# Performance work log

Hardware: AMD Instinct MI355X
Metric: run time of the kernel (lower is better)

Reference implementation:

```python
import jax, jax.numpy as jnp
import numpy as np

N_POINTS = 32768
N_PRIMS = 2048
C_LIGHT = 299792458.0


def setup_inputs() -> dict:
    key = jax.random.key(0)
    k1, k2, k3, k4, k5 = jax.random.split(key, 5)
    # query points and primitive centers in a ~room-scale scene (metres)
    query_points = jax.random.normal(k1, (N_POINTS, 3), dtype=jnp.float32) * 2.0
    positions = jax.random.normal(k2, (N_PRIMS, 3), dtype=jnp.float32) * 2.0
    # diagonal anisotropic scales, kept away from zero for stability
    scales = jax.random.uniform(k3, (N_PRIMS, 3), dtype=jnp.float32, minval=0.1, maxval=1.0)
    amplitudes = jax.random.uniform(k4, (N_PRIMS,), dtype=jnp.float32, minval=0.0, maxval=1.0)
    phases = jax.random.uniform(k5, (N_PRIMS,), dtype=jnp.float32, minval=-np.pi, maxval=np.pi)
    return {
        "query_points": query_points,
        "positions": positions,
        "scales": scales,
        "amplitudes": amplitudes,
        "phases": phases,
        "frequency": 2400000000,  # 2.4 GHz
    }


def reference(query_points, positions, scales, amplitudes, phases, frequency):
    """Batched equivalent of: field = sum_p primitive_p.evaluate(query_points, frequency).

    Each complex Gaussian primitive contributes
        a_p * exp(-0.5 * (x-mu_p)^T diag(1/s_p^2) (x-mu_p)) * exp(i*(phi_p + k*|x-mu_p|))
    with wavenumber k = 2*pi*f/c. All pairwise terms are expressed as GEMMs.
    """
    f = jnp.float32(frequency)
    k_wave = jnp.float32(2.0 * np.pi) * f / jnp.float32(C_LIGHT)

    inv_var = 1.0 / (scales * scales)                      # [P,3]
    x2 = query_points * query_points                       # [N,3]
    mu2w = jnp.sum(positions * positions * inv_var, axis=1)  # [P]
    # Mahalanobis distance^2: sum_d (x_d-mu_d)^2 / s_d^2, expanded into GEMMs
    maha = (x2 @ inv_var.T
            - 2.0 * (query_points @ (positions * inv_var).T)
            + mu2w[None, :])                               # [N,P]
    maha = jnp.maximum(maha, 0.0)
    # Euclidean distance for the propagation phase
    d2 = (jnp.sum(x2, axis=1, keepdims=True)
          - 2.0 * (query_points @ positions.T)
          + jnp.sum(positions * positions, axis=1)[None, :])  # [N,P]
    r = jnp.sqrt(jnp.maximum(d2, 1e-12))

    w = amplitudes[None, :] * jnp.exp(-0.5 * maha)         # [N,P] real envelope
    ph = phases[None, :] + k_wave * r                      # [N,P] total phase
    field = jax.lax.complex(jnp.sum(w * jnp.cos(ph), axis=1),
                            jnp.sum(w * jnp.sin(ph), axis=1))  # [N] complex64
    return field
```

## Files before the change

kernel.cpp:

```cpp
#include <hip/hip_runtime.h>
#include <math.h>

#define NPOINTS 32768
#define NPRIMS  2048
#define BLK     256
#define PBLK    (NPOINTS / BLK)
#define NSPLIT  16

typedef float v2f __attribute__((ext_vector_type(2)));

struct PrimPair { float4 q0, q1, q2, q3; };

__device__ __forceinline__ float read_freq(const void* p) {
    const unsigned* w = (const unsigned*)p;
    unsigned lo = w[0];
    float ff = __uint_as_float(lo);
    if (ff >= 1.0e5f && ff <= 1.0e13f) return ff;
    if (lo != 0u) return (float)lo;
    double d = *(const double*)p;
    if (d >= 1.0e5 && d <= 1.0e13) return (float)d;
    unsigned long long v = ((unsigned long long)w[1] << 32) | lo;
    return (float)v;
}

__global__ __launch_bounds__(BLK) void prep_kernel(
        const float* __restrict__ pos,
        const float* __restrict__ scl,
        const float* __restrict__ amp,
        const float* __restrict__ ph,
        PrimPair* __restrict__ pp) {
    int j = blockIdx.x * blockDim.x + threadIdx.x;
    if (j >= NPRIMS / 2) return;
    const float KE     = -0.72134752044448169f;
    const float INV2PI =  0.15915494309189535f;
    int p0 = 2 * j, p1 = 2 * j + 1;
    float s0x = scl[3*p0+0], s0y = scl[3*p0+1], s0z = scl[3*p0+2];
    float s1x = scl[3*p1+0], s1y = scl[3*p1+1], s1z = scl[3*p1+2];
    PrimPair P;
    P.q0 = make_float4(pos[3*p0+0], pos[3*p1+0], pos[3*p0+1], pos[3*p1+1]);
    P.q1 = make_float4(pos[3*p0+2], pos[3*p1+2], amp[p0], amp[p1]);
    P.q2 = make_float4(KE / (s0x*s0x), KE / (s1x*s1x), KE / (s0y*s0y), KE / (s1y*s1y));
    P.q3 = make_float4(KE / (s0z*s0z), KE / (s1z*s1z), ph[p0] * INV2PI, ph[p1] * INV2PI);
    pp[j] = P;
}

__global__ __launch_bounds__(BLK) void field_kernel(
        const float* __restrict__ qp,
        const PrimPair* __restrict__ pp,
        const void* __restrict__ freq_p,
        float2* __restrict__ part) {
    const int n = blockIdx.x * BLK + threadIdx.x;
    const float x = qp[3*n+0], y = qp[3*n+1], z = qp[3*n+2];
    const float kr = read_freq(freq_p) / 299792458.0f;

    constexpr int PAIRS = (NPRIMS / NSPLIT) / 2;
    const int base = blockIdx.y * PAIRS;

    v2f re = {0.0f, 0.0f}, im = {0.0f, 0.0f};
    const v2f xx = {x, x}, yy = {y, y}, zz = {z, z};
    const v2f kr2 = {kr, kr};
    const v2f eps2 = {1e-12f, 1e-12f};

    #pragma unroll 4
    for (int j = 0; j < PAIRS; ++j) {
        PrimPair P = pp[base + j];
        v2f mux = {P.q0.x, P.q0.y}, muy = {P.q0.z, P.q0.w};
        v2f muz = {P.q1.x, P.q1.y}, am2 = {P.q1.z, P.q1.w};
        v2f gx  = {P.q2.x, P.q2.y}, gy  = {P.q2.z, P.q2.w};
        v2f gz  = {P.q3.x, P.q3.y}, ph2 = {P.q3.z, P.q3.w};

        v2f dx = xx - mux, dy = yy - muy, dz = zz - muz;
        v2f t0 = dx * dx, t1 = dy * dy, t2 = dz * dz;
        v2f e  = t0 * gx + t1 * gy + t2 * gz;
        v2f d2 = t0 + t1 + t2;
        d2 = __builtin_elementwise_max(d2, eps2);

        float r0 = __builtin_amdgcn_sqrtf(d2.x);
        float r1 = __builtin_amdgcn_sqrtf(d2.y);
        float e0 = __builtin_amdgcn_exp2f(e.x);
        float e1 = __builtin_amdgcn_exp2f(e.y);
        v2f r2 = {r0, r1};
        v2f ex = {e0, e1};
        v2f w2 = am2 * ex;
        v2f tp = kr2 * r2 + ph2;
        float f0 = __builtin_amdgcn_fractf(tp.x);
        float f1 = __builtin_amdgcn_fractf(tp.y);
        float s0 = __builtin_amdgcn_sinf(f0);
        float s1 = __builtin_amdgcn_sinf(f1);
        float c0 = __builtin_amdgcn_cosf(f0);
        float c1 = __builtin_amdgcn_cosf(f1);
        v2f s2 = {s0, s1}, c2 = {c0, c1};
        re += w2 * c2;
        im += w2 * s2;
    }

    part[(size_t)blockIdx.y * NPOINTS + n] = make_float2(re.x + re.y, im.x + im.y);
}

__global__ __launch_bounds__(BLK) void reduce_kernel(const float2* __restrict__ part,
                                                     float* __restrict__ out) {
    int n = blockIdx.x * blockDim.x + threadIdx.x;
    float re = 0.0f, im = 0.0f;
    #pragma unroll
    for (int s = 0; s < NSPLIT; ++s) {
        float2 v = part[(size_t)s * NPOINTS + n];
        re += v.x; im += v.y;
    }
    out[n]           = re;
    out[NPOINTS + n] = im;
}

__global__ __launch_bounds__(BLK) void field_fallback(
        const float* __restrict__ qp,
        const float* __restrict__ pos,
        const float* __restrict__ scl,
        const float* __restrict__ amp,
        const float* __restrict__ ph,
        const void*  __restrict__ freq_p,
        float*       __restrict__ out) {
    __shared__ float4 sA[128];
    __shared__ float4 sB[128];
    const int n = blockIdx.x * BLK + threadIdx.x;
    const float x = qp[3*n+0], y = qp[3*n+1], z = qp[3*n+2];
    const float kr = read_freq(freq_p) / 299792458.0f;
    const float KE = -0.72134752044448169f, INV2PI = 0.15915494309189535f;
    float re = 0.0f, im = 0.0f;
    for (int tile = 0; tile < NPRIMS / 128; ++tile) {
        __syncthreads();
        if (threadIdx.x < 128) {
            int p = tile * 128 + threadIdx.x;
            float sx = scl[3*p+0], sy = scl[3*p+1], sz = scl[3*p+2];
            sA[threadIdx.x] = make_float4(pos[3*p+0], pos[3*p+1], pos[3*p+2], amp[p]);
            sB[threadIdx.x] = make_float4(KE/(sx*sx), KE/(sy*sy), KE/(sz*sz), ph[p]*INV2PI);
        }
        __syncthreads();
        #pragma unroll 8
        for (int p = 0; p < 128; ++p) {
            float4 a = sA[p];
            float4 b = sB[p];
            float dx = x - a.x, dy = y - a.y, dz = z - a.z;
            float t0 = dx*dx, t1 = dy*dy, t2 = dz*dz;
            float e  = fmaf(t0, b.x, fmaf(t1, b.y, t2 * b.z));
            float d2 = t0 + t1 + t2;
            float r  = __builtin_amdgcn_sqrtf(fmaxf(d2, 1e-12f));
            float w  = a.w * __builtin_amdgcn_exp2f(e);
            float tp = __builtin_amdgcn_fractf(fmaf(kr, r, b.w));
            float s  = __builtin_amdgcn_sinf(tp);
            float c  = __builtin_amdgcn_cosf(tp);
            re = fmaf(w, c, re);
            im = fmaf(w, s, im);
        }
    }
    out[n]           = re;
    out[NPOINTS + n] = im;
}

extern "C" void kernel_launch(void* const* d_in, const int* in_sizes, int n_in,
                              void* d_out, int out_size, void* d_ws, size_t ws_size,
                              hipStream_t stream) {
    const float* qp  = (const float*)d_in[0];
    const float* pos = (const float*)d_in[1];
    const float* scl = (const float*)d_in[2];
    const float* amp = (const float*)d_in[3];
    const float* ph  = (const float*)d_in[4];
    const void*  fq  = d_in[5];
    float* out = (float*)d_out;

    const size_t packed_bytes = (size_t)(NPRIMS / 2) * sizeof(PrimPair);
    const size_t part_bytes   = (size_t)NSPLIT * NPOINTS * sizeof(float2);

    if (ws_size >= packed_bytes + part_bytes) {
        PrimPair* pp   = (PrimPair*)d_ws;
        float2*   part = (float2*)((char*)d_ws + packed_bytes);
        prep_kernel<<<dim3((NPRIMS/2 + BLK - 1) / BLK), dim3(BLK), 0, stream>>>(pos, scl, amp, ph, pp);
        field_kernel<<<dim3(PBLK, NSPLIT), dim3(BLK), 0, stream>>>(qp, pp, fq, part);
        reduce_kernel<<<dim3(NPOINTS / BLK), dim3(BLK), 0, stream>>>(part, out);
    } else {
        field_fallback<<<dim3(PBLK), dim3(BLK), 0, stream>>>(qp, pos, scl, amp, ph, fq, out);
    }
}
```

Before: 47.27 us.

## Process two points per thread and replace hardware sin/cos with packed polynomials

Each thread now evaluates two query points against each primitive pair, reusing every loaded PrimPair across both points and halving the grid. The hardware transcendental sin/cos (fract plus v_sin/v_cos on the quarter-rate unit) is replaced by packed minimax polynomials in revolutions, evaluated with packed FMA on full-rate ALUs. The next PrimPair is software-prefetched one iteration ahead. The trade-off is more registers, fewer waves in the grid, and more VALU instructions per term, with a possible small accuracy change from the polynomial.

```diff
diff --git a/kernel.cpp b/kernel.cpp
--- a/kernel.cpp
+++ b/kernel.cpp
@@ -4,7 +4,9 @@
 #define NPOINTS 32768
 #define NPRIMS  2048
 #define BLK     256
-#define PBLK    (NPOINTS / BLK)
+#define PPT     2
+#define PTS_BLK (BLK * PPT)
+#define PBLK    (NPOINTS / PTS_BLK)
 #define NSPLIT  16
 
 typedef float v2f __attribute__((ext_vector_type(2)));
@@ -44,57 +46,97 @@
     pp[j] = P;
 }
 
+__device__ __forceinline__ void pk_sincos_rev(v2f tp, v2f& s, v2f& c) {
+    const v2f S1 = {-41.34170224039976f, -41.34170224039976f};
+    const v2f S2 = { 81.60524927607504f,  81.60524927607504f};
+    const v2f S3 = {-76.70585975306136f, -76.70585975306136f};
+    const v2f S4 = { 42.05869394489765f,  42.05869394489765f};
+    const v2f S5 = {-15.094642576822123f,-15.094642576822123f};
+    const v2f S6 = {  3.8199525848482824f, 3.8199525848482824f};
+    const v2f S0 = {  6.283185307179586f,  6.283185307179586f};
+    const v2f C1 = {-19.739208802178716f,-19.739208802178716f};
+    const v2f C2 = { 64.93939402266829f,  64.93939402266829f};
+    const v2f C3 = {-85.45681720669372f, -85.45681720669372f};
+    const v2f C4 = { 60.24464137187665f,  60.24464137187665f};
+    const v2f C5 = {-26.426256783358706f,-26.426256783358706f};
+    const v2f C6 = {  7.903536371318467f,  7.903536371318467f};
+    const v2f C7 = { -1.714370232222585f, -1.714370232222585f};
+    const v2f ONE = {1.0f, 1.0f};
+
+    v2f n  = {__builtin_rintf(tp.x), __builtin_rintf(tp.y)};
+    v2f v  = tp - n;
+    v2f w  = v * v;
+    v2f ps = __builtin_elementwise_fma(w, S6, S5);
+    ps = __builtin_elementwise_fma(w, ps, S4);
+    ps = __builtin_elementwise_fma(w, ps, S3);
+    ps = __builtin_elementwise_fma(w, ps, S2);
+    ps = __builtin_elementwise_fma(w, ps, S1);
+    ps = __builtin_elementwise_fma(w, ps, S0);
+    s  = v * ps;
+    v2f pc = __builtin_elementwise_fma(w, C7, C6);
+    pc = __builtin_elementwise_fma(w, pc, C5);
+    pc = __builtin_elementwise_fma(w, pc, C4);
+    pc = __builtin_elementwise_fma(w, pc, C3);
+    pc = __builtin_elementwise_fma(w, pc, C2);
+    pc = __builtin_elementwise_fma(w, pc, C1);
+    c  = __builtin_elementwise_fma(w, pc, ONE);
+}
+
+__device__ __forceinline__ void eval_pair(const PrimPair& P,
+                                          v2f xx, v2f yy, v2f zz, v2f kr2,
+                                          v2f& re, v2f& im) {
+    v2f mux = {P.q0.x, P.q0.y}, muy = {P.q0.z, P.q0.w};
+    v2f muz = {P.q1.x, P.q1.y}, am2 = {P.q1.z, P.q1.w};
+    v2f gx  = {P.q2.x, P.q2.y}, gy  = {P.q2.z, P.q2.w};
+    v2f gz  = {P.q3.x, P.q3.y}, ph2 = {P.q3.z, P.q3.w};
+
+    v2f dx = xx - mux, dy = yy - muy, dz = zz - muz;
+    v2f t0 = dx * dx, t1 = dy * dy, t2 = dz * dz;
+    v2f e  = t0 * gx + t1 * gy + t2 * gz;
+    v2f d2 = t0 + t1 + t2;
+    d2 = __builtin_elementwise_max(d2, (v2f){1e-12f, 1e-12f});
+
+    v2f r2 = {__builtin_amdgcn_sqrtf(d2.x), __builtin_amdgcn_sqrtf(d2.y)};
+    v2f ex = {__builtin_amdgcn_exp2f(e.x),  __builtin_amdgcn_exp2f(e.y)};
+    v2f w2 = am2 * ex;
+    v2f tp = __builtin_elementwise_fma(kr2, r2, ph2);
+    v2f s2, c2;
+    pk_sincos_rev(tp, s2, c2);
+    re = __builtin_elementwise_fma(w2, c2, re);
+    im = __builtin_elementwise_fma(w2, s2, im);
+}
+
 __global__ __launch_bounds__(BLK) void field_kernel(
         const float* __restrict__ qp,
         const PrimPair* __restrict__ pp,
         const void* __restrict__ freq_p,
         float2* __restrict__ part) {
-    const int n = blockIdx.x * BLK + threadIdx.x;
-    const float x = qp[3*n+0], y = qp[3*n+1], z = qp[3*n+2];
+    const int n0 = blockIdx.x * PTS_BLK + threadIdx.x;
+    const int n1 = n0 + BLK;
     const float kr = read_freq(freq_p) / 299792458.0f;
+    const v2f kr2 = {kr, kr};
+
+    const v2f xxa = {qp[3*n0+0], qp[3*n0+0]}, yya = {qp[3*n0+1], qp[3*n0+1]},
+              zza = {qp[3*n0+2], qp[3*n0+2]};
+    const v2f xxb = {qp[3*n1+0], qp[3*n1+0]}, yyb = {qp[3*n1+1], qp[3*n1+1]},
+              zzb = {qp[3*n1+2], qp[3*n1+2]};
 
     constexpr int PAIRS = (NPRIMS / NSPLIT) / 2;
     const int base = blockIdx.y * PAIRS;
 
-    v2f re = {0.0f, 0.0f}, im = {0.0f, 0.0f};
-    const v2f xx = {x, x}, yy = {y, y}, zz = {z, z};
-    const v2f kr2 = {kr, kr};
-    const v2f eps2 = {1e-12f, 1e-12f};
-
-    #pragma unroll 4
+    v2f reA = {0.0f, 0.0f}, imA = {0.0f, 0.0f};
+    v2f reB = {0.0f, 0.0f}, imB = {0.0f, 0.0f};
+
+    PrimPair cur = pp[base];
     for (int j = 0; j < PAIRS; ++j) {
-        PrimPair P = pp[base + j];
-        v2f mux = {P.q0.x, P.q0.y}, muy = {P.q0.z, P.q0.w};
-        v2f muz = {P.q1.x, P.q1.y}, am2 = {P.q1.z, P.q1.w};
-        v2f gx  = {P.q2.x, P.q2.y}, gy  = {P.q2.z, P.q2.w};
-        v2f gz  = {P.q3.x, P.q3.y}, ph2 = {P.q3.z, P.q3.w};
-
-        v2f dx = xx - mux, dy = yy - muy, dz = zz - muz;
-        v2f t0 = dx * dx, t1 = dy * dy, t2 = dz * dz;
-        v2f e  = t0 * gx + t1 * gy + t2 * gz;
-        v2f d2 = t0 + t1 + t2;
-        d2 = __builtin_elementwise_max(d2, eps2);
-
-        float r0 = __builtin_amdgcn_sqrtf(d2.x);
-        float r1 = __builtin_amdgcn_sqrtf(d2.y);
-        float e0 = __builtin_amdgcn_exp2f(e.x);
-        float e1 = __builtin_amdgcn_exp2f(e.y);
-        v2f r2 = {r0, r1};
-        v2f ex = {e0, e1};
-        v2f w2 = am2 * ex;
-        v2f tp = kr2 * r2 + ph2;
-        float f0 = __builtin_amdgcn_fractf(tp.x);
-        float f1 = __builtin_amdgcn_fractf(tp.y);
-        float s0 = __builtin_amdgcn_sinf(f0);
-        float s1 = __builtin_amdgcn_sinf(f1);
-        float c0 = __builtin_amdgcn_cosf(f0);
-        float c1 = __builtin_amdgcn_cosf(f1);
-        v2f s2 = {s0, s1}, c2 = {c0, c1};
-        re += w2 * c2;
-        im += w2 * s2;
-    }
-
-    part[(size_t)blockIdx.y * NPOINTS + n] = make_float2(re.x + re.y, im.x + im.y);
+        PrimPair nxt = pp[base + ((j + 1) & (PAIRS - 1))];
+        eval_pair(cur, xxa, yya, zza, kr2, reA, imA);
+        eval_pair(cur, xxb, yyb, zzb, kr2, reB, imB);
+        cur = nxt;
+    }
+
+    part[(size_t)blockIdx.y * NPOINTS + n0] = make_float2(reA.x + reA.y, imA.x + imA.y);
+    part[(size_t)blockIdx.y * NPOINTS + n1] = make_float2(reB.x + reB.y, imB.x + imB.y);
 }
 
 __global__ __launch_bounds__(BLK) void reduce_kernel(const float2* __restrict__ part,
@@ -176,6 +218,6 @@
         field_kernel<<<dim3(PBLK, NSPLIT), dim3(BLK), 0, stream>>>(qp, pp, fq, part);
         reduce_kernel<<<dim3(NPOINTS / BLK), dim3(BLK), 0, stream>>>(part, out);
     } else {
-        field_fallback<<<dim3(PBLK), dim3(BLK), 0, stream>>>(qp, pos, scl, amp, ph, fq, out);
-    }
-}
+        field_fallback<<<dim3(NPOINTS / BLK), dim3(BLK), 0, stream>>>(qp, pos, scl, amp, ph, fq, out);
+    }
+}
```

After: 63.84 us. 1.35x slower.
